# Kernel tuning notes

Hardware: AMD Instinct MI355X
Metric: run time of the kernel (lower is better)

## Reference

```python
import jax, jax.numpy as jnp
import numpy as np

N_NODES = 50000
N_EDGES = 625000
HIDDEN = 128
NUM_GRAPHS = 128
EPS = 1e-5


def setup_inputs() -> dict:
    key = jax.random.key(0)
    ks = jax.random.split(key, 8)
    node = jax.random.normal(ks[0], (N_NODES, HIDDEN), dtype=jnp.float32)
    edge_index = jax.random.randint(ks[1], (2, N_EDGES), 0, N_NODES, dtype=jnp.int64)
    edge_attr = jax.random.uniform(ks[2], (N_EDGES,), dtype=jnp.float32)
    batch_ptr = jnp.sort(jax.random.randint(ks[3], (N_NODES,), 0, NUM_GRAPHS, dtype=jnp.int64))
    # GCNConv linear: weight [out,in], bias [out]
    W = jax.random.normal(ks[4], (HIDDEN, HIDDEN), dtype=jnp.float32) * (1.0 / np.sqrt(HIDDEN))
    b = jnp.zeros((HIDDEN,), dtype=jnp.float32)
    # GraphNorm params
    gn_weight = 1.0 + 0.02 * jax.random.normal(ks[5], (HIDDEN,), dtype=jnp.float32)
    gn_bias = 0.05 * jax.random.normal(ks[6], (HIDDEN,), dtype=jnp.float32)
    gn_mean_scale = 1.0 + 0.02 * jax.random.normal(ks[7], (HIDDEN,), dtype=jnp.float32)
    return {"node": node, "edge_index": edge_index, "edge_attr": edge_attr,
            "batch_ptr": batch_ptr, "W": W, "b": b,
            "gn_weight": gn_weight, "gn_bias": gn_bias, "gn_mean_scale": gn_mean_scale}


def _gcn_conv(x, src, dst, w, W, b):
    n = x.shape[0]
    # add self loops with weight 1
    loop = jnp.arange(n, dtype=src.dtype)
    src = jnp.concatenate([src, loop])
    dst = jnp.concatenate([dst, loop])
    w = jnp.concatenate([w, jnp.ones((n,), dtype=w.dtype)])
    # symmetric degree normalization (degrees at target nodes)
    deg = jax.ops.segment_sum(w, dst, num_segments=n)
    dinv = jnp.where(deg > 0, jax.lax.rsqrt(deg), 0.0)
    norm = dinv[src] * w * dinv[dst]  # [E+n]
    h = x @ W.T  # [n, d]
    msg = norm[:, None] * h[src]  # gather + scale
    out = jax.ops.segment_sum(msg, dst, num_segments=n)  # scatter-add
    return out + b


def _graph_norm(x, batch, weight, bias, mean_scale):
    cnt = jax.ops.segment_sum(jnp.ones((x.shape[0],), x.dtype), batch, num_segments=NUM_GRAPHS)
    cnt = jnp.maximum(cnt, 1.0)[:, None]
    mean = jax.ops.segment_sum(x, batch, num_segments=NUM_GRAPHS) / cnt
    centered = x - mean_scale * mean[batch]
    var = jax.ops.segment_sum(centered * centered, batch, num_segments=NUM_GRAPHS) / cnt
    inv_std = jax.lax.rsqrt(var + EPS)[batch]
    return weight * centered * inv_std + bias


def reference(node, edge_index, edge_attr, batch_ptr, W, b, gn_weight, gn_bias, gn_mean_scale):
    src, dst = edge_index[0], edge_index[1]
    h = _gcn_conv(node, src, dst, edge_attr, W, b)
    h = _graph_norm(h, batch_ptr, gn_weight, gn_bias, gn_mean_scale)
    return jax.nn.relu(h)
```

## Files before the change

### kernel.cpp

```cpp
#include <hip/hip_runtime.h>

#define N_NODES    50000
#define N_EDGES    625000
#define HIDDEN     128
#define NUM_GRAPHS 128
#define EPS_GN     1e-5f
#define FIXSCALE   1048576.0f
#define NGEMM_BLK  782
#define NHIST_BLK  611
#define CPAD       8

typedef __bf16 bf16x8 __attribute__((ext_vector_type(8)));
typedef float  f32x4  __attribute__((ext_vector_type(4)));
typedef unsigned short u16x8 __attribute__((ext_vector_type(8)));
typedef unsigned long long u64;

__device__ inline unsigned short f2b(float f) {
    __bf16 b = (__bf16)f;
    return __builtin_bit_cast(unsigned short, b);
}
__device__ inline float b2f(unsigned short u) {
    unsigned int x = ((unsigned int)u) << 16;
    return __builtin_bit_cast(float, x);
}

#define HB_OFF     0
#define CNT64_OFF  3200000
#define DINV_OFF   4000000
#define GSTART_OFF 4082768
#define ROWS_OFF   4083000
#define BSUM_OFF   4133100
#define BOFF_OFF   4133400
#define EPACK_OFF  4133700
#define SLOT_OFF   5383700
#define WB_OFF     6008700
#define TMP_OFF    6020000
#undef TMP_OFF
#define TMP_OFF    5383700
#undef WB_OFF
#define WB_OFF     4050000

__global__ void prep(const float* __restrict__ W, unsigned short* __restrict__ wb,
                     uint4* __restrict__ cntz) {
    int i = blockIdx.x * 256 + threadIdx.x;
    if (i < 800000 / 4) cntz[i] = make_uint4(0u, 0u, 0u, 0u);
    if (i < HIDDEN * HIDDEN) wb[i] = f2b(W[i]);
}

__global__ __launch_bounds__(256) void gemm_hist(const float* __restrict__ x,
                                                 const unsigned short* __restrict__ wb,
                                                 unsigned short* __restrict__ hb,
                                                 const int* __restrict__ dst,
                                                 const float* __restrict__ w,
                                                 u64* __restrict__ cnt64,
                                                 unsigned int* __restrict__ slot) {
    if (blockIdx.x >= NGEMM_BLK) {
        int base = (blockIdx.x - NGEMM_BLK) * 256 + threadIdx.x;
        if (base * 4 >= N_EDGES) return;
        int4   d4 = ((const int4*)dst)[base];
        float4 w4 = ((const float4*)w)[base];
        unsigned int fx0 = (unsigned int)(w4.x * FIXSCALE + 0.5f);
        unsigned int fx1 = (unsigned int)(w4.y * FIXSCALE + 0.5f);
        unsigned int fx2 = (unsigned int)(w4.z * FIXSCALE + 0.5f);
        unsigned int fx3 = (unsigned int)(w4.w * FIXSCALE + 0.5f);
        u64 o0 = atomicAdd(&cnt64[(size_t)d4.x * CPAD], (1ULL << 32) | (u64)fx0);
        u64 o1 = atomicAdd(&cnt64[(size_t)d4.y * CPAD], (1ULL << 32) | (u64)fx1);
        u64 o2 = atomicAdd(&cnt64[(size_t)d4.z * CPAD], (1ULL << 32) | (u64)fx2);
        u64 o3 = atomicAdd(&cnt64[(size_t)d4.w * CPAD], (1ULL << 32) | (u64)fx3);
        uint4 s4;
        s4.x = (unsigned int)(o0 >> 32);
        s4.y = (unsigned int)(o1 >> 32);
        s4.z = (unsigned int)(o2 >> 32);
        s4.w = (unsigned int)(o3 >> 32);
        ((uint4*)slot)[base] = s4;
        return;
    }
    const int wave = threadIdx.x >> 6;
    const int lane = threadIdx.x & 63;
    const int row0 = blockIdx.x * 64 + wave * 16;
    const int r  = lane & 15;
    const int ko = (lane >> 4) * 8;
    f32x4 acc[8];
#pragma unroll
    for (int t = 0; t < 8; ++t) { acc[t][0] = 0.f; acc[t][1] = 0.f; acc[t][2] = 0.f; acc[t][3] = 0.f; }
    int arow = row0 + r;
    if (arow >= N_NODES) arow = N_NODES - 1;
    const size_t abase = (size_t)arow * HIDDEN + ko;
#pragma unroll
    for (int kt = 0; kt < HIDDEN; kt += 32) {
        float4 a0 = *(const float4*)(x + abase + kt);
        float4 a1 = *(const float4*)(x + abase + kt + 4);
        bf16x8 a;
        a[0] = (__bf16)a0.x; a[1] = (__bf16)a0.y; a[2] = (__bf16)a0.z; a[3] = (__bf16)a0.w;
        a[4] = (__bf16)a1.x; a[5] = (__bf16)a1.y; a[6] = (__bf16)a1.z; a[7] = (__bf16)a1.w;
#pragma unroll
        for (int t = 0; t < 8; ++t) {
            bf16x8 b = *(const bf16x8*)(wb + (size_t)(t * 16 + r) * HIDDEN + kt + ko);
            acc[t] = __builtin_amdgcn_mfma_f32_16x16x32_bf16(a, b, acc[t], 0, 0, 0);
        }
    }
    const int orow = row0 + (lane >> 4) * 4;
#pragma unroll
    for (int t = 0; t < 8; ++t) {
#pragma unroll
        for (int j = 0; j < 4; ++j) {
            int rr = orow + j;
            if (rr < N_NODES) hb[(size_t)rr * HIDDEN + t * 16 + r] = f2b(acc[t][j]);
        }
    }
}

__global__ void scan_partial(const u64* __restrict__ cnt64, int* __restrict__ bsum,
                             float* __restrict__ dinv,
                             const int* __restrict__ batch, int* __restrict__ gstart) {
    __shared__ int red[256];
    int i = blockIdx.x * 256 + threadIdx.x;
    int c = 0;
    if (i < N_NODES) {
        u64 v = cnt64[(size_t)i * CPAD];
        c = (int)(v >> 32);
        dinv[i] = rsqrtf(1.0f + (float)(unsigned int)v * (1.0f / FIXSCALE));
        int b0 = batch[i];
        int prev = (i == 0) ? -1 : batch[i - 1];
        for (int g = prev + 1; g <= b0; ++g) gstart[g] = i;
        if (i == N_NODES - 1) {
            for (int g = b0 + 1; g <= NUM_GRAPHS; ++g) gstart[g] = N_NODES;
        }
    }
    red[threadIdx.x] = c;
    __syncthreads();
    for (int off = 128; off > 0; off >>= 1) {
        if (threadIdx.x < off) red[threadIdx.x] += red[threadIdx.x + off];
        __syncthreads();
    }
    if (threadIdx.x == 0) bsum[blockIdx.x] = red[0];
}

__global__ void scan_bsums(const int* __restrict__ bsum, int* __restrict__ boff, int nblocks) {
    __shared__ int s[256];
    int t = threadIdx.x;
    int v0 = (t < nblocks) ? bsum[t] : 0;
    s[t] = v0;
    __syncthreads();
    for (int off = 1; off < 256; off <<= 1) {
        int v = (t >= off) ? s[t - off] : 0;
        __syncthreads();
        s[t] += v;
        __syncthreads();
    }
    boff[t] = s[t] - v0;
}

__global__ void scan_emit(const u64* __restrict__ cnt64, const int* __restrict__ boff,
                          int* __restrict__ rowstart) {
    __shared__ int s[256];
    int t = threadIdx.x;
    int i = blockIdx.x * 256 + t;
    int v0 = (i < N_NODES) ? (int)(cnt64[(size_t)i * CPAD] >> 32) : 0;
    s[t] = v0;
    __syncthreads();
    for (int off = 1; off < 256; off <<= 1) {
        int v = (t >= off) ? s[t - off] : 0;
        __syncthreads();
        s[t] += v;
        __syncthreads();
    }
    if (i < N_NODES) rowstart[i] = boff[blockIdx.x] + s[t] - v0;
    if (i == N_NODES) rowstart[N_NODES] = N_EDGES;
}

__global__ void csr_fill(const int* __restrict__ src, const int* __restrict__ dst,
                         const float* __restrict__ w, const float* __restrict__ dinv,
                         const int* __restrict__ rowstart, const unsigned int* __restrict__ slot,
                         u64* __restrict__ epack) {
    int base = blockIdx.x * blockDim.x + threadIdx.x;
    if (base * 4 >= N_EDGES) return;
    int4   s4 = ((const int4*)src)[base];
    int4   d4 = ((const int4*)dst)[base];
    float4 w4 = ((const float4*)w)[base];
    uint4  r4 = ((const uint4*)slot)[base];
    float nm0 = dinv[s4.x] * w4.x * dinv[d4.x];
    float nm1 = dinv[s4.y] * w4.y * dinv[d4.y];
    float nm2 = dinv[s4.z] * w4.z * dinv[d4.z];
    float nm3 = dinv[s4.w] * w4.w * dinv[d4.w];
    epack[rowstart[d4.x] + (int)r4.x] = (u64)(unsigned int)s4.x | ((u64)__float_as_uint(nm0) << 32);
    epack[rowstart[d4.y] + (int)r4.y] = (u64)(unsigned int)s4.y | ((u64)__float_as_uint(nm1) << 32);
    epack[rowstart[d4.z] + (int)r4.z] = (u64)(unsigned int)s4.z | ((u64)__float_as_uint(nm2) << 32);
    epack[rowstart[d4.w] + (int)r4.w] = (u64)(unsigned int)s4.w | ((u64)__float_as_uint(nm3) << 32);
}

__global__ __launch_bounds__(256) void gather_fused(const unsigned short* __restrict__ hb,
                                                    const int* __restrict__ rowstart,
                                                    const u64* __restrict__ epack,
                                                    const float* __restrict__ dinv,
                                                    const float* __restrict__ b,
                                                    unsigned short* __restrict__ tmp) {
    const int t = threadIdx.x;
    const int n = blockIdx.x * 16 + (t >> 4);
    if (n >= N_NODES) return;
    const int c8 = (t & 15) * 8;
    const int s0 = rowstart[n];
    const int e0 = rowstart[n + 1];
    const float di = dinv[n];
    const float sl = di * di;
    float acc[8];
    {
        u16x8 hv = *(const u16x8*)(hb + (size_t)n * HIDDEN + c8);
#pragma unroll
        for (int j = 0; j < 8; ++j) acc[j] = sl * b2f(hv[j]);
    }
    int p = s0;
    for (; p + 2 <= e0; p += 2) {
        u64 e1 = epack[p];
        u64 e2 = epack[p + 1];
        int   s1 = (int)(unsigned int)e1;
        float n1 = __uint_as_float((unsigned int)(e1 >> 32));
        int   sg2 = (int)(unsigned int)e2;
        float n2 = __uint_as_float((unsigned int)(e2 >> 32));
        u16x8 v1 = *(const u16x8*)(hb + (size_t)s1 * HIDDEN + c8);
        u16x8 v2 = *(const u16x8*)(hb + (size_t)sg2 * HIDDEN + c8);
#pragma unroll
        for (int j = 0; j < 8; ++j) acc[j] = fmaf(n1, b2f(v1[j]), acc[j]);
#pragma unroll
        for (int j = 0; j < 8; ++j) acc[j] = fmaf(n2, b2f(v2[j]), acc[j]);
    }
    if (p < e0) {
        u64 e1 = epack[p];
        int   s1 = (int)(unsigned int)e1;
        float n1 = __uint_as_float((unsigned int)(e1 >> 32));
        u16x8 v1 = *(const u16x8*)(hb + (size_t)s1 * HIDDEN + c8);
#pragma unroll
        for (int j = 0; j < 8; ++j) acc[j] = fmaf(n1, b2f(v1[j]), acc[j]);
    }
    float4 b0 = *(const float4*)(b + c8);
    float4 b1 = *(const float4*)(b + c8 + 4);
    u16x8 o;
    o[0] = f2b(acc[0] + b0.x); o[1] = f2b(acc[1] + b0.y);
    o[2] = f2b(acc[2] + b0.z); o[3] = f2b(acc[3] + b0.w);
    o[4] = f2b(acc[4] + b1.x); o[5] = f2b(acc[5] + b1.y);
    o[6] = f2b(acc[6] + b1.z); o[7] = f2b(acc[7] + b1.w);
    *(u16x8*)(tmp + (size_t)n * HIDDEN + c8) = o;
}

__global__ __launch_bounds__(256) void stats_apply(const unsigned short* __restrict__ tmp,
                                                   const int* __restrict__ gstart,
                                                   const float* __restrict__ ms,
                                                   const float* __restrict__ gw,
                                                   const float* __restrict__ gb,
                                                   float* __restrict__ out) {
    const int g = blockIdx.x >> 2;
    const int q = blockIdx.x & 3;
    const int l = threadIdx.x & 31;
    const int c = q * 32 + l;
    const int r = threadIdx.x >> 5;
    const int s = gstart[g];
    const int e = gstart[g + 1];
    float sum = 0.f, sq = 0.f;
    for (int n = s + r; n < e; n += 8) {
        float v = b2f(tmp[(size_t)n * HIDDEN + c]);
        sum += v;
        sq = fmaf(v, v, sq);
    }
    __shared__ float ssum[8][32], ssq[8][32];
    __shared__ float sA[32], sS[32];
    ssum[r][l] = sum;
    ssq[r][l]  = sq;
    __syncthreads();
    if (r == 0) {
#pragma unroll
        for (int i = 1; i < 8; ++i) { sum += ssum[i][l]; sq += ssq[i][l]; }
        float cnt  = (float)max(e - s, 1);
        float mean = sum / cnt;
        float m2   = sq / cnt;
        float msv  = ms[c];
        float var  = fmaxf(m2 - mean * mean * msv * (2.f - msv), 0.f);
        float a    = gw[c] * rsqrtf(var + EPS_GN);
        sA[l] = a;
        sS[l] = gb[c] - a * msv * mean;
    }
    __syncthreads();
    float a  = sA[l];
    float sh = sS[l];
    for (int n = s + r; n < e; n += 8) {
        float v = b2f(tmp[(size_t)n * HIDDEN + c]);
        out[(size_t)n * HIDDEN + c] = fmaxf(fmaf(a, v, sh), 0.f);
    }
}

extern "C" void kernel_launch(void* const* d_in, const int* in_sizes, int n_in,
                              void* d_out, int out_size, void* d_ws, size_t ws_size,
                              hipStream_t stream) {
    const float* node  = (const float*)d_in[0];
    const int*   ei    = (const int*)d_in[1];
    const float* eattr = (const float*)d_in[2];
    const int*   batch = (const int*)d_in[3];
    const float* W     = (const float*)d_in[4];
    const float* b     = (const float*)d_in[5];
    const float* gnw   = (const float*)d_in[6];
    const float* gnb   = (const float*)d_in[7];
    const float* gnms  = (const float*)d_in[8];
    float* out = (float*)d_out;
    float* ws  = (float*)d_ws;

    const int* src = ei;
    const int* dst = ei + N_EDGES;

    unsigned short* hb = (unsigned short*)(ws + HB_OFF);
    u64*   cnt64   = (u64*)(ws + CNT64_OFF);
    float* dinv    = ws + DINV_OFF;
    int*   gstart  = (int*)(ws + GSTART_OFF);
    int*   rowstart= (int*)(ws + ROWS_OFF);
    int*   bsum    = (int*)(ws + BSUM_OFF);
    int*   boff    = (int*)(ws + BOFF_OFF);
    u64*   epack   = (u64*)(ws + EPACK_OFF);
    unsigned int* slot = (unsigned int*)(ws + SLOT_OFF);
    unsigned short* wb = (unsigned short*)(ws + WB_OFF);
    unsigned short* tmp = (unsigned short*)(ws + TMP_OFF);

    const int NB = (N_NODES + 255) / 256;

    prep<<<(200000 + 255) / 256, 256, 0, stream>>>(W, wb, (uint4*)cnt64);
    gemm_hist<<<NGEMM_BLK + NHIST_BLK, 256, 0, stream>>>(node, wb, hb, dst, eattr, cnt64, slot);
    scan_partial<<<NB, 256, 0, stream>>>(cnt64, bsum, dinv, batch, gstart);
    scan_bsums<<<1, 256, 0, stream>>>(bsum, boff, NB);
    scan_emit<<<NB, 256, 0, stream>>>(cnt64, boff, rowstart);
    csr_fill<<<(N_EDGES / 4 + 255) / 256, 256, 0, stream>>>(src, dst, eattr, dinv, rowstart, slot, epack);
    gather_fused<<<(N_NODES + 15) / 16, 256, 0, stream>>>(hb, rowstart, epack, dinv, b, tmp);
    stats_apply<<<NUM_GRAPHS * 4, 256, 0, stream>>>(tmp, gstart, gnms, gnw, gnb, out);

    (void)in_sizes; (void)n_in; (void)out_size; (void)ws_size;
}
```

Baseline: 128.3 us.

## Compact degree counters, merge scan kernels, widen histogram and gather unrolling

Removes the 8-way padding on the per-node 64-bit degree/count counters, so the zeroing pass and the counter reads touch an eighth of the memory. Folds the block-sum scan into scan_emit so each block rescans the block sums itself, which drops one kernel launch. Histogram threads now process 8 edges each, halving the histogram block count, and the gather loop is unrolled by 4 to keep more row loads in flight. Without padding, atomics on neighbouring nodes can share cache lines, which may add contention in the atomic stage.

```diff
diff --git a/kernel.cpp b/kernel.cpp
--- a/kernel.cpp
+++ b/kernel.cpp
@@ -7,8 +7,8 @@
 #define EPS_GN     1e-5f
 #define FIXSCALE   1048576.0f
 #define NGEMM_BLK  782
-#define NHIST_BLK  611
-#define CPAD       8
+#define NHIST_BLK  306
+#define NB_SCAN    196
 
 typedef __bf16 bf16x8 __attribute__((ext_vector_type(8)));
 typedef float  f32x4  __attribute__((ext_vector_type(4)));
@@ -26,24 +26,21 @@
 
 #define HB_OFF     0
 #define CNT64_OFF  3200000
-#define DINV_OFF   4000000
-#define GSTART_OFF 4082768
-#define ROWS_OFF   4083000
-#define BSUM_OFF   4133100
-#define BOFF_OFF   4133400
-#define EPACK_OFF  4133700
-#define SLOT_OFF   5383700
-#define WB_OFF     6008700
-#define TMP_OFF    6020000
+#define DINV_OFF   3300000
+#define WB_OFF     3352000
+#define GSTART_OFF 3362000
+#define ROWS_OFF   3363000
+#define BSUM_OFF   3414000
+#define EPACK_OFF  3414100
+#define SLOT_OFF   4664100
+#define TMP_OFF    5289104
 #undef TMP_OFF
-#define TMP_OFF    5383700
-#undef WB_OFF
-#define WB_OFF     4050000
+#define TMP_OFF    4664100
 
 __global__ void prep(const float* __restrict__ W, unsigned short* __restrict__ wb,
                      uint4* __restrict__ cntz) {
     int i = blockIdx.x * 256 + threadIdx.x;
-    if (i < 800000 / 4) cntz[i] = make_uint4(0u, 0u, 0u, 0u);
+    if (i < 100000 / 4) cntz[i] = make_uint4(0u, 0u, 0u, 0u);
     if (i < HIDDEN * HIDDEN) wb[i] = f2b(W[i]);
 }
 
@@ -56,23 +53,32 @@
                                                  unsigned int* __restrict__ slot) {
     if (blockIdx.x >= NGEMM_BLK) {
         int base = (blockIdx.x - NGEMM_BLK) * 256 + threadIdx.x;
-        if (base * 4 >= N_EDGES) return;
-        int4   d4 = ((const int4*)dst)[base];
-        float4 w4 = ((const float4*)w)[base];
-        unsigned int fx0 = (unsigned int)(w4.x * FIXSCALE + 0.5f);
-        unsigned int fx1 = (unsigned int)(w4.y * FIXSCALE + 0.5f);
-        unsigned int fx2 = (unsigned int)(w4.z * FIXSCALE + 0.5f);
-        unsigned int fx3 = (unsigned int)(w4.w * FIXSCALE + 0.5f);
-        u64 o0 = atomicAdd(&cnt64[(size_t)d4.x * CPAD], (1ULL << 32) | (u64)fx0);
-        u64 o1 = atomicAdd(&cnt64[(size_t)d4.y * CPAD], (1ULL << 32) | (u64)fx1);
-        u64 o2 = atomicAdd(&cnt64[(size_t)d4.z * CPAD], (1ULL << 32) | (u64)fx2);
-        u64 o3 = atomicAdd(&cnt64[(size_t)d4.w * CPAD], (1ULL << 32) | (u64)fx3);
-        uint4 s4;
-        s4.x = (unsigned int)(o0 >> 32);
-        s4.y = (unsigned int)(o1 >> 32);
-        s4.z = (unsigned int)(o2 >> 32);
-        s4.w = (unsigned int)(o3 >> 32);
-        ((uint4*)slot)[base] = s4;
+        if (base * 8 >= N_EDGES) return;
+        int4   dA = ((const int4*)dst)[base * 2];
+        int4   dB = ((const int4*)dst)[base * 2 + 1];
+        float4 wA = ((const float4*)w)[base * 2];
+        float4 wB = ((const float4*)w)[base * 2 + 1];
+        uint4 sA, sB;
+        {
+            unsigned int fx = (unsigned int)(wA.x * FIXSCALE + 0.5f);
+            sA.x = (unsigned int)(atomicAdd(&cnt64[dA.x], (1ULL << 32) | (u64)fx) >> 32);
+            fx = (unsigned int)(wA.y * FIXSCALE + 0.5f);
+            sA.y = (unsigned int)(atomicAdd(&cnt64[dA.y], (1ULL << 32) | (u64)fx) >> 32);
+            fx = (unsigned int)(wA.z * FIXSCALE + 0.5f);
+            sA.z = (unsigned int)(atomicAdd(&cnt64[dA.z], (1ULL << 32) | (u64)fx) >> 32);
+            fx = (unsigned int)(wA.w * FIXSCALE + 0.5f);
+            sA.w = (unsigned int)(atomicAdd(&cnt64[dA.w], (1ULL << 32) | (u64)fx) >> 32);
+            fx = (unsigned int)(wB.x * FIXSCALE + 0.5f);
+            sB.x = (unsigned int)(atomicAdd(&cnt64[dB.x], (1ULL << 32) | (u64)fx) >> 32);
+            fx = (unsigned int)(wB.y * FIXSCALE + 0.5f);
+            sB.y = (unsigned int)(atomicAdd(&cnt64[dB.y], (1ULL << 32) | (u64)fx) >> 32);
+            fx = (unsigned int)(wB.z * FIXSCALE + 0.5f);
+            sB.z = (unsigned int)(atomicAdd(&cnt64[dB.z], (1ULL << 32) | (u64)fx) >> 32);
+            fx = (unsigned int)(wB.w * FIXSCALE + 0.5f);
+            sB.w = (unsigned int)(atomicAdd(&cnt64[dB.w], (1ULL << 32) | (u64)fx) >> 32);
+        }
+        ((uint4*)slot)[base * 2]     = sA;
+        ((uint4*)slot)[base * 2 + 1] = sB;
         return;
     }
     const int wave = threadIdx.x >> 6;
@@ -117,7 +123,7 @@
     int i = blockIdx.x * 256 + threadIdx.x;
     int c = 0;
     if (i < N_NODES) {
-        u64 v = cnt64[(size_t)i * CPAD];
+        u64 v = cnt64[i];
         c = (int)(v >> 32);
         dinv[i] = rsqrtf(1.0f + (float)(unsigned int)v * (1.0f / FIXSCALE));
         int b0 = batch[i];
@@ -136,10 +142,22 @@
     if (threadIdx.x == 0) bsum[blockIdx.x] = red[0];
 }
 
-__global__ void scan_bsums(const int* __restrict__ bsum, int* __restrict__ boff, int nblocks) {
+__global__ void scan_emit(const u64* __restrict__ cnt64, const int* __restrict__ bsum,
+                          int* __restrict__ rowstart) {
+    __shared__ int sb[256];
     __shared__ int s[256];
     int t = threadIdx.x;
-    int v0 = (t < nblocks) ? bsum[t] : 0;
+    sb[t] = (t < NB_SCAN) ? bsum[t] : 0;
+    __syncthreads();
+    for (int off = 1; off < 256; off <<= 1) {
+        int v = (t >= off) ? sb[t - off] : 0;
+        __syncthreads();
+        sb[t] += v;
+        __syncthreads();
+    }
+    int boff = (blockIdx.x == 0) ? 0 : sb[blockIdx.x - 1];
+    int i = blockIdx.x * 256 + t;
+    int v0 = (i < N_NODES) ? (int)(cnt64[i] >> 32) : 0;
     s[t] = v0;
     __syncthreads();
     for (int off = 1; off < 256; off <<= 1) {
@@ -148,24 +166,7 @@
         s[t] += v;
         __syncthreads();
     }
-    boff[t] = s[t] - v0;
-}
-
-__global__ void scan_emit(const u64* __restrict__ cnt64, const int* __restrict__ boff,
-                          int* __restrict__ rowstart) {
-    __shared__ int s[256];
-    int t = threadIdx.x;
-    int i = blockIdx.x * 256 + t;
-    int v0 = (i < N_NODES) ? (int)(cnt64[(size_t)i * CPAD] >> 32) : 0;
-    s[t] = v0;
-    __syncthreads();
-    for (int off = 1; off < 256; off <<= 1) {
-        int v = (t >= off) ? s[t - off] : 0;
-        __syncthreads();
-        s[t] += v;
-        __syncthreads();
-    }
-    if (i < N_NODES) rowstart[i] = boff[blockIdx.x] + s[t] - v0;
+    if (i < N_NODES) rowstart[i] = boff + s[t] - v0;
     if (i == N_NODES) rowstart[N_NODES] = N_EDGES;
 }
 
@@ -210,25 +211,37 @@
         for (int j = 0; j < 8; ++j) acc[j] = sl * b2f(hv[j]);
     }
     int p = s0;
-    for (; p + 2 <= e0; p += 2) {
+    for (; p + 4 <= e0; p += 4) {
         u64 e1 = epack[p];
         u64 e2 = epack[p + 1];
-        int   s1 = (int)(unsigned int)e1;
+        u64 e3 = epack[p + 2];
+        u64 e4 = epack[p + 3];
+        int   x1 = (int)(unsigned int)e1;
+        int   x2 = (int)(unsigned int)e2;
+        int   x3 = (int)(unsigned int)e3;
+        int   x4 = (int)(unsigned int)e4;
         float n1 = __uint_as_float((unsigned int)(e1 >> 32));
-        int   sg2 = (int)(unsigned int)e2;
         float n2 = __uint_as_float((unsigned int)(e2 >> 32));
-        u16x8 v1 = *(const u16x8*)(hb + (size_t)s1 * HIDDEN + c8);
-        u16x8 v2 = *(const u16x8*)(hb + (size_t)sg2 * HIDDEN + c8);
+        float n3 = __uint_as_float((unsigned int)(e3 >> 32));
+        float n4 = __uint_as_float((unsigned int)(e4 >> 32));
+        u16x8 v1 = *(const u16x8*)(hb + (size_t)x1 * HIDDEN + c8);
+        u16x8 v2 = *(const u16x8*)(hb + (size_t)x2 * HIDDEN + c8);
+        u16x8 v3 = *(const u16x8*)(hb + (size_t)x3 * HIDDEN + c8);
+        u16x8 v4 = *(const u16x8*)(hb + (size_t)x4 * HIDDEN + c8);
 #pragma unroll
         for (int j = 0; j < 8; ++j) acc[j] = fmaf(n1, b2f(v1[j]), acc[j]);
 #pragma unroll
         for (int j = 0; j < 8; ++j) acc[j] = fmaf(n2, b2f(v2[j]), acc[j]);
-    }
-    if (p < e0) {
+#pragma unroll
+        for (int j = 0; j < 8; ++j) acc[j] = fmaf(n3, b2f(v3[j]), acc[j]);
+#pragma unroll
+        for (int j = 0; j < 8; ++j) acc[j] = fmaf(n4, b2f(v4[j]), acc[j]);
+    }
+    for (; p < e0; ++p) {
         u64 e1 = epack[p];
-        int   s1 = (int)(unsigned int)e1;
+        int   x1 = (int)(unsigned int)e1;
         float n1 = __uint_as_float((unsigned int)(e1 >> 32));
-        u16x8 v1 = *(const u16x8*)(hb + (size_t)s1 * HIDDEN + c8);
+        u16x8 v1 = *(const u16x8*)(hb + (size_t)x1 * HIDDEN + c8);
 #pragma unroll
         for (int j = 0; j < 8; ++j) acc[j] = fmaf(n1, b2f(v1[j]), acc[j]);
     }
@@ -308,22 +321,18 @@
     unsigned short* hb = (unsigned short*)(ws + HB_OFF);
     u64*   cnt64   = (u64*)(ws + CNT64_OFF);
     float* dinv    = ws + DINV_OFF;
+    unsigned short* wb = (unsigned short*)(ws + WB_OFF);
     int*   gstart  = (int*)(ws + GSTART_OFF);
     int*   rowstart= (int*)(ws + ROWS_OFF);
     int*   bsum    = (int*)(ws + BSUM_OFF);
-    int*   boff    = (int*)(ws + BOFF_OFF);
     u64*   epack   = (u64*)(ws + EPACK_OFF);
     unsigned int* slot = (unsigned int*)(ws + SLOT_OFF);
-    unsigned short* wb = (unsigned short*)(ws + WB_OFF);
     unsigned short* tmp = (unsigned short*)(ws + TMP_OFF);
 
-    const int NB = (N_NODES + 255) / 256;
-
-    prep<<<(200000 + 255) / 256, 256, 0, stream>>>(W, wb, (uint4*)cnt64);
+    prep<<<98, 256, 0, stream>>>(W, wb, (uint4*)cnt64);
     gemm_hist<<<NGEMM_BLK + NHIST_BLK, 256, 0, stream>>>(node, wb, hb, dst, eattr, cnt64, slot);
-    scan_partial<<<NB, 256, 0, stream>>>(cnt64, bsum, dinv, batch, gstart);
-    scan_bsums<<<1, 256, 0, stream>>>(bsum, boff, NB);
-    scan_emit<<<NB, 256, 0, stream>>>(cnt64, boff, rowstart);
+    scan_partial<<<NB_SCAN, 256, 0, stream>>>(cnt64, bsum, dinv, batch, gstart);
+    scan_emit<<<NB_SCAN, 256, 0, stream>>>(cnt64, bsum, rowstart);
     csr_fill<<<(N_EDGES / 4 + 255) / 256, 256, 0, stream>>>(src, dst, eattr, dinv, rowstart, slot, epack);
     gather_fused<<<(N_NODES + 15) / 16, 256, 0, stream>>>(hb, rowstart, epack, dinv, b, tmp);
     stats_apply<<<NUM_GRAPHS * 4, 256, 0, stream>>>(tmp, gstart, gnms, gnw, gnb, out);
```

Result: faster. 124.5 us (-3.0%).
